# Kernel tuning notes

Measured on AMD Instinct MI355X. Metric: run time of the kernel, lower is better.

The kernel has to match this reference:

```python
import jax, jax.numpy as jnp
import numpy as np

N_NODES_TOTAL = 61440   # B*30
NODES = 30              # per-graph node count (forced by view(-1, 30*128))
E = 491520
IN_CH = 12
CHANS = [128, 512, 128]
KSIZE = 3
FC_OUT = 72             # 12 * 6


def setup_inputs() -> dict:
    key = jax.random.key(0)
    ks = jax.random.split(key, 24)
    d = {}
    d['x'] = jax.random.normal(ks[0], (N_NODES_TOTAL, IN_CH), dtype=jnp.float32)
    d['edge_index'] = jax.random.randint(ks[1], (2, E), 0, N_NODES_TOTAL, dtype=jnp.int64)
    # GCNConv(12, 12): PyG Linear weight [out, in] + bias
    d['gcn_w'] = jax.random.normal(ks[2], (12, 12), dtype=jnp.float32) * (1.0 / np.sqrt(12))
    d['gcn_b'] = jnp.zeros((12,), dtype=jnp.float32)
    # TCN: 3 TemporalBlocks, each uses conv1 (k=3, dilated causal) + 1x1 downsample
    in_c = IN_CH
    for i, out_c in enumerate(CHANS):
        d[f'conv_w{i}'] = jax.random.normal(ks[3 + 4 * i], (out_c, in_c, KSIZE), dtype=jnp.float32) * 0.01
        d[f'conv_b{i}'] = jnp.zeros((out_c,), dtype=jnp.float32)
        d[f'down_w{i}'] = jax.random.normal(ks[4 + 4 * i], (out_c, in_c, 1), dtype=jnp.float32) * 0.01
        d[f'down_b{i}'] = jnp.zeros((out_c,), dtype=jnp.float32)
        in_c = out_c
    d['fc_w'] = jax.random.normal(ks[20], (FC_OUT, CHANS[-1] * NODES), dtype=jnp.float32) * (1.0 / np.sqrt(CHANS[-1] * NODES))
    d['fc_b'] = jnp.zeros((FC_OUT,), dtype=jnp.float32)
    return d


def gcn_conv(x, edge_index, w, b):
    # PyG GCNConv: h = x W^T, add self-loops, sym normalize, scatter-add, + bias
    n = x.shape[0]
    h = x @ w.T
    loop = jnp.arange(n, dtype=edge_index.dtype)
    src = jnp.concatenate([edge_index[0], loop])
    dst = jnp.concatenate([edge_index[1], loop])
    deg = jax.ops.segment_sum(jnp.ones(src.shape[0], dtype=h.dtype), dst, num_segments=n)
    dinv = jnp.where(deg > 0, jax.lax.rsqrt(deg), 0.0)
    norm = dinv[src] * dinv[dst]                       # [E+N]
    out = jax.ops.segment_sum(norm[:, None] * h[src], dst, num_segments=n)
    return out + b


def causal_conv1d(x, w, b, dilation):
    # torch Conv1d(pad=(k-1)*d both sides) + Chomp1d((k-1)*d) == left-pad causal conv
    k = w.shape[-1]
    pad = (k - 1) * dilation
    y = jax.lax.conv_general_dilated(
        x, w, window_strides=(1,), padding=[(pad, 0)],
        rhs_dilation=(dilation,), dimension_numbers=('NCH', 'OIH', 'NCH'))
    return y + b[None, :, None]


def reference(x, edge_index, gcn_w, gcn_b,
              conv_w0, conv_b0, down_w0, down_b0,
              conv_w1, conv_b1, down_w1, down_b1,
              conv_w2, conv_b2, down_w2, down_b2,
              fc_w, fc_b):
    X = gcn_conv(x, edge_index, gcn_w, gcn_b)          # [B*30, 12]
    X = X.reshape(-1, NODES, IN_CH).transpose(0, 2, 1)  # [B, 12, 30]
    blocks = [(conv_w0, conv_b0, down_w0, down_b0),
              (conv_w1, conv_b1, down_w1, down_b1),
              (conv_w2, conv_b2, down_w2, down_b2)]
    for i, (cw, cb, dw, db) in enumerate(blocks):
        dil = 3 ** i
        out = jax.nn.relu(causal_conv1d(X, cw, cb, dil))
        res = causal_conv1d(X, dw, db, 1)              # 1x1 downsample (always in!=out here)
        X = jax.nn.relu(out + res)
    T = jax.nn.relu(X)                                  # [B, 128, 30]
    T = T.reshape(T.shape[0], -1)                       # [B, 3840], channel-major like torch flatten
    return T @ fc_w.T + fc_b                            # [B, 72]
```

## Files before the change

### kernel.cpp

```cpp
#include <hip/hip_runtime.h>
#include <hip/hip_bf16.h>

#define N_NODES 61440
#define NEDGE   491520
#define BATCH   2048
#define TT      30
#define C1      128
#define C2      512
#define C3      128
#define FCK     3840
#define MAXDEG  40

typedef float floatx16 __attribute__((ext_vector_type(16)));
typedef __bf16 bfrag   __attribute__((ext_vector_type(8)));

static __device__ __forceinline__ unsigned short f2bf(float f) {
    unsigned u = __float_as_uint(f);
    u = u + 0x7fffu + ((u >> 16) & 1u);
    return (unsigned short)(u >> 16);
}
static __device__ __forceinline__ bfrag ldf(const void* p) { return *(const bfrag*)p; }
#define MFMA(a, b, c) __builtin_amdgcn_mfma_f32_32x32x16_bf16(a, b, c, 0, 0, 0)

__global__ void k_edges_repack(
        const int* __restrict__ e32, int* __restrict__ cnt,
        unsigned short* __restrict__ eidx,
        const float* __restrict__ cw0, const float* __restrict__ dw0,
        const float* __restrict__ cw1, const float* __restrict__ dw1,
        const float* __restrict__ cw2, const float* __restrict__ dw2,
        const float* __restrict__ fcw,
        float* __restrict__ w0T, float* __restrict__ d0T,
        unsigned short* __restrict__ W1f, unsigned short* __restrict__ D1f,
        unsigned short* __restrict__ W2f, unsigned short* __restrict__ D2f,
        unsigned short* __restrict__ FCWf) {
    if (blockIdx.x < 1920) {
        int i = blockIdx.x * 256 + threadIdx.x;
        bool is64 = (e32[1] == 0) & (e32[3] == 0) & (e32[5] == 0) & (e32[7] == 0);
        int s, d;
        if (is64) { s = e32[2 * i]; d = e32[2 * (NEDGE + i)]; }
        else      { s = e32[i];     d = e32[NEDGE + i]; }
        int slot = atomicAdd(&cnt[d], 1);
        if (slot < MAXDEG) eidx[slot * N_NODES + d] = (unsigned short)s;
        return;
    }
    int i = (blockIdx.x - 1920) * 256 + threadIdx.x;
    if (i < 36 * 128) { int oc = i & 127, r = i >> 7; w0T[i] = cw0[oc * 36 + r]; }
    if (i < 12 * 128) { int oc = i & 127, ic = i >> 7; d0T[i] = dw0[oc * 12 + ic]; }
    if (i < 196608) {
        int pos = i & 511, f = i >> 9;
        int lane = pos >> 3, e = pos & 7;
        int oct = f & 15, q = (f >> 4) & 7, tap = f >> 7;
        int oc = oct * 32 + (lane & 31), ic = q * 16 + (lane >> 5) * 8 + e;
        W1f[i] = f2bf(cw1[(oc * 128 + ic) * 3 + tap]);
    } else if (i < 262144) {
        int j = i - 196608;
        int pos = j & 511, f = j >> 9;
        int lane = pos >> 3, e = pos & 7;
        int oct = f & 15, q = f >> 4;
        int oc = oct * 32 + (lane & 31), ic = q * 16 + (lane >> 5) * 8 + e;
        D1f[j] = f2bf(dw1[oc * 128 + ic]);
    } else if (i < 458752) {
        int j = i - 262144;
        int pos = j & 511, f = j >> 9;
        int lane = pos >> 3, e = pos & 7;
        int oct = f & 3, q = (f >> 2) & 31, tap = f >> 7;
        int oc = oct * 32 + (lane & 31), ic = q * 16 + (lane >> 5) * 8 + e;
        W2f[j] = f2bf(cw2[(oc * 512 + ic) * 3 + tap]);
    } else if (i < 524288) {
        int j = i - 458752;
        int pos = j & 511, f = j >> 9;
        int lane = pos >> 3, e = pos & 7;
        int oct = f & 3, q = f >> 2;
        int oc = oct * 32 + (lane & 31), ic = q * 16 + (lane >> 5) * 8 + e;
        D2f[j] = f2bf(dw2[oc * 512 + ic]);
    } else if (i < 892928) {
        int j = i - 524288;
        int pos = j & 511, f = j >> 9;
        int lane = pos >> 3, e = pos & 7;
        int oct = f % 3, q = f / 3;
        int o = oct * 32 + (lane & 31);
        int k = q * 16 + (lane >> 5) * 8 + e;
        float v = (o < 72) ? fcw[o * 3840 + (k & 127) * 30 + (k >> 7)] : 0.f;
        FCWf[j] = f2bf(v);
    }
}

__global__ __launch_bounds__(256) void k_block0(
        const float* __restrict__ x, const int* __restrict__ cnt,
        const unsigned short* __restrict__ eidx,
        const float* __restrict__ gw, const float* __restrict__ gb,
        const float* __restrict__ w0T, const float* __restrict__ d0T,
        const float* __restrict__ cb0, const float* __restrict__ db0,
        unsigned short* __restrict__ X1b) {
    __shared__ float wl[36 * 128];
    __shared__ float dl[12 * 128];
    __shared__ float cbl[128], dbl[128];
    __shared__ float gwl[144], gbl[12];
    __shared__ float aL[120][12];
    __shared__ float x0[4 * TT * 12];
    __shared__ __align__(16) unsigned short st[2][TT * 136];
    int tid = threadIdx.x;
    int b0 = blockIdx.x * 4;
    for (int i = tid; i < 36 * 128; i += 256) wl[i] = w0T[i];
    for (int i = tid; i < 12 * 128; i += 256) dl[i] = d0T[i];
    if (tid < 128) { cbl[tid] = cb0[tid]; dbl[tid] = db0[tid]; }
    if (tid < 144) gwl[tid] = gw[tid];
    if (tid >= 144 && tid < 156) gbl[tid - 144] = gb[tid - 144];

    {
        int th = tid & 127;
        int grp = tid >> 7;
        if (th < 120) {
            size_t n = (size_t)b0 * TT + th;
            int ne = cnt[n]; if (ne > MAXDEG) ne = MAXDEG;
            float a0 = 0.f, a1 = 0.f, a2 = 0.f, a3 = 0.f, a4 = 0.f, a5 = 0.f;
            for (int j = 0; j < ne; j++) {
                int s = eidx[j * N_NODES + n];
                float di = rsqrtf(1.0f + (float)cnt[s]);
                const float2* xp = (const float2*)(x + (size_t)s * 12 + grp * 6);
                float2 p0 = xp[0], p1 = xp[1], p2 = xp[2];
                a0 += di * p0.x; a1 += di * p0.y;
                a2 += di * p1.x; a3 += di * p1.y;
                a4 += di * p2.x; a5 += di * p2.y;
            }
            float* ap = &aL[th][grp * 6];
            ap[0] = a0; ap[1] = a1; ap[2] = a2; ap[3] = a3; ap[4] = a4; ap[5] = a5;
        }
    }
    __syncthreads();

    if (tid < 120) {
        size_t n = (size_t)b0 * TT + tid;
        float di = rsqrtf(1.0f + (float)cnt[n]);
        float d2 = di * di;
        const float4* xp = (const float4*)(x + n * 12);
        float u[12];
        #pragma unroll
        for (int q = 0; q < 3; q++) {
            float4 xv = xp[q];
            u[q*4+0] = di * aL[tid][q*4+0] + d2 * xv.x;
            u[q*4+1] = di * aL[tid][q*4+1] + d2 * xv.y;
            u[q*4+2] = di * aL[tid][q*4+2] + d2 * xv.z;
            u[q*4+3] = di * aL[tid][q*4+3] + d2 * xv.w;
        }
        #pragma unroll
        for (int c = 0; c < 12; c++) {
            float acc = gbl[c];
            #pragma unroll
            for (int j = 0; j < 12; j++) acc += u[j] * gwl[c * 12 + j];
            x0[tid * 12 + c] = acc;
        }
    }
    __syncthreads();

    int oc = tid & 127, half = tid >> 7;
    float cb = cbl[oc], db = dbl[oc];
    for (int bi = 0; bi < 2; bi++) {
        int bl = bi * 2 + half;
        const float* xb = x0 + bl * (TT * 12);
        float conv[TT], res[TT];
        #pragma unroll
        for (int t = 0; t < TT; t++) { conv[t] = 0.f; res[t] = 0.f; }
        #pragma unroll
        for (int ic = 0; ic < 12; ic++) {
            float w0v = wl[(ic * 3 + 0) * 128 + oc];
            float w1v = wl[(ic * 3 + 1) * 128 + oc];
            float w2v = wl[(ic * 3 + 2) * 128 + oc];
            float dv  = dl[ic * 128 + oc];
            #pragma unroll
            for (int t = 0; t < TT; t++) {
                float xv = xb[t * 12 + ic];
                conv[t] += w2v * xv;
                if (t + 1 < TT) conv[t + 1] += w1v * xv;
                if (t + 2 < TT) conv[t + 2] += w0v * xv;
                res[t] += dv * xv;
            }
        }
        #pragma unroll
        for (int t = 0; t < TT; t++) {
            float o1 = fmaxf(conv[t] + cb, 0.f);
            st[half][t * 136 + oc] = f2bf(fmaxf(o1 + res[t] + db, 0.f));
        }
        __syncthreads();
        for (int idx = tid; idx < 2 * TT * 16; idx += 256) {
            int h = idx / (TT * 16), rem = idx - h * (TT * 16);
            int row = rem >> 4, seg = rem & 15;
            *(uint4*)(X1b + (size_t)((b0 + bi * 2 + h) * TT + row) * 128 + seg * 8) =
                *(const uint4*)(&st[h][row * 136 + seg * 8]);
        }
        __syncthreads();
    }
}

__global__ __launch_bounds__(512, 2) void k_tcn12(
        const unsigned short* __restrict__ X1b,
        const unsigned short* __restrict__ W1f, const unsigned short* __restrict__ D1f,
        const float* __restrict__ cb1, const float* __restrict__ db1,
        const unsigned short* __restrict__ W2f, const unsigned short* __restrict__ D2f,
        const float* __restrict__ cb2, const float* __restrict__ db2,
        unsigned short* __restrict__ X3b) {
    __shared__ __align__(16) unsigned short X1l[61 * 136];
    __shared__ __align__(16) unsigned short X2l[61 * 520];
    const int tid  = threadIdx.x;
    const int lane = tid & 63;
    const int wave = tid >> 6;
    const int tcol = lane & 31;
    const int half = lane >> 5;
    const int b0 = blockIdx.x * 2;

    auto ldw1 = [&](bfrag* dst, int oct, int qc) {
        #pragma unroll
        for (int tap = 0; tap < 3; tap++)
            #pragma unroll
            for (int qq = 0; qq < 4; qq++)
                dst[tap * 4 + qq] =
                    ldf(W1f + (((tap * 8 + qc * 4 + qq) * 16 + oct) << 9) + lane * 8);
        #pragma unroll
        for (int qq = 0; qq < 4; qq++)
            dst[12 + qq] = ldf(D1f + (((qc * 4 + qq) * 16 + oct) << 9) + lane * 8);
    };
    auto ldw2 = [&](bfrag* dst, int oct, int qc) {
        #pragma unroll
        for (int tap = 0; tap < 3; tap++)
            #pragma unroll
            for (int qq = 0; qq < 4; qq++)
                dst[tap * 4 + qq] =
                    ldf(W2f + (((tap * 32 + qc * 4 + qq) * 4 + oct) << 9) + lane * 8);
        #pragma unroll
        for (int qq = 0; qq < 4; qq++)
            dst[12 + qq] = ldf(D2f + (((qc * 4 + qq) * 4 + oct) << 9) + lane * 8);
    };

    for (int idx = tid; idx < 960; idx += 512) {
        int row = idx >> 4, seg = idx & 15;
        *(uint4*)(X1l + row * 136 + seg * 8) =
            *(const uint4*)(X1b + ((size_t)(b0 * 30 + row) << 7) + seg * 8);
    }
    if (tid < 17) *(uint4*)(X1l + 60 * 136 + tid * 8) = make_uint4(0, 0, 0, 0);
    if (tid < 65) *(uint4*)(X2l + 60 * 520 + tid * 8) = make_uint4(0, 0, 0, 0);
    __syncthreads();

    {
        bfrag wf[2][16];
        ldw1(wf[0], wave, 0);
        floatx16 accc[2], accd[2];
        #pragma unroll
        for (int s = 0; s < 4; s++) {
            const int qc = s & 1;
            const int oct = (s >> 1) * 8 + wave;
            if (qc == 0) { accc[0] = 0; accc[1] = 0; accd[0] = 0; accd[1] = 0; }
            if (s < 3)
                ldw1(wf[(s + 1) & 1], ((s + 1) >> 1) * 8 + wave, (s + 1) & 1);
            #pragma unroll
            for (int bl = 0; bl < 2; bl++) {
                bfrag bx[3][4];
                #pragma unroll
                for (int si = 0; si < 3; si++) {
                    int trow = tcol - si * 3;
                    const unsigned short* rp = ((unsigned)trow < 30u)
                        ? (X1l + (bl * 30 + trow) * 136) : (X1l + 60 * 136);
                    #pragma unroll
                    for (int qq = 0; qq < 4; qq++)
                        bx[si][qq] = ldf(rp + (qc * 4 + qq) * 16 + half * 8);
                }
                #pragma unroll
                for (int qq = 0; qq < 4; qq++) {
                    accc[bl] = MFMA(wf[s & 1][8 + qq],  bx[0][qq], accc[bl]);
                    accc[bl] = MFMA(wf[s & 1][4 + qq],  bx[1][qq], accc[bl]);
                    accc[bl] = MFMA(wf[s & 1][qq],      bx[2][qq], accc[bl]);
                    accd[bl] = MFMA(wf[s & 1][12 + qq], bx[0][qq], accd[bl]);
                }
            }
            if (qc == 1 && tcol < 30) {
                #pragma unroll
                for (int bl = 0; bl < 2; bl++) {
                    unsigned short* wp = X2l + (bl * 30 + tcol) * 520 + oct * 32 + half * 4;
                    #pragma unroll
                    for (int gi = 0; gi < 4; gi++) {
                        int ocb = oct * 32 + half * 4 + gi * 8;
                        float4 cbv = *(const float4*)(cb1 + ocb);
                        float4 dbv = *(const float4*)(db1 + ocb);
                        float v0 = fmaxf(fmaxf(accc[bl][gi*4+0] + cbv.x, 0.f) + accd[bl][gi*4+0] + dbv.x, 0.f);
                        float v1 = fmaxf(fmaxf(accc[bl][gi*4+1] + cbv.y, 0.f) + accd[bl][gi*4+1] + dbv.y, 0.f);
                        float v2 = fmaxf(fmaxf(accc[bl][gi*4+2] + cbv.z, 0.f) + accd[bl][gi*4+2] + dbv.z, 0.f);
                        float v3 = fmaxf(fmaxf(accc[bl][gi*4+3] + cbv.w, 0.f) + accd[bl][gi*4+3] + dbv.w, 0.f);
                        unsigned p0 = (unsigned)f2bf(v0) | ((unsigned)f2bf(v1) << 16);
                        unsigned p1 = (unsigned)f2bf(v2) | ((unsigned)f2bf(v3) << 16);
                        *(uint2*)(wp + gi * 8) = make_uint2(p0, p1);
                    }
                }
            }
        }
    }
    __syncthreads();

    {
        const int oct = wave & 3;
        const int bl  = wave >> 2;
        bfrag wf[2][16];
        ldw2(wf[0], oct, 0);
        floatx16 accc, accd;
        accc = 0; accd = 0;
        #pragma unroll
        for (int qc = 0; qc < 8; qc++) {
            if (qc < 7) ldw2(wf[(qc + 1) & 1], oct, qc + 1);
            bfrag bx[3][4];
            #pragma unroll
            for (int si = 0; si < 3; si++) {
                int trow = tcol - si * 9;
                const unsigned short* rp = ((unsigned)trow < 30u)
                    ? (X2l + (bl * 30 + trow) * 520) : (X2l + 60 * 520);
                #pragma unroll
                for (int qq = 0; qq < 4; qq++)
                    bx[si][qq] = ldf(rp + (qc * 4 + qq) * 16 + half * 8);
            }
            #pragma unroll
            for (int qq = 0; qq < 4; qq++) {
                accc = MFMA(wf[qc & 1][8 + qq],  bx[0][qq], accc);
                accc = MFMA(wf[qc & 1][4 + qq],  bx[1][qq], accc);
                accc = MFMA(wf[qc & 1][qq],      bx[2][qq], accc);
                accd = MFMA(wf[qc & 1][12 + qq], bx[0][qq], accd);
            }
        }
        if (tcol < 30) {
            unsigned short* wp = X1l + (bl * 30 + tcol) * 136 + oct * 32 + half * 4;
            #pragma unroll
            for (int gi = 0; gi < 4; gi++) {
                int ocb = oct * 32 + half * 4 + gi * 8;
                float4 cbv = *(const float4*)(cb2 + ocb);
                float4 dbv = *(const float4*)(db2 + ocb);
                float v0 = fmaxf(fmaxf(accc[gi*4+0] + cbv.x, 0.f) + accd[gi*4+0] + dbv.x, 0.f);
                float v1 = fmaxf(fmaxf(accc[gi*4+1] + cbv.y, 0.f) + accd[gi*4+1] + dbv.y, 0.f);
                float v2 = fmaxf(fmaxf(accc[gi*4+2] + cbv.z, 0.f) + accd[gi*4+2] + dbv.z, 0.f);
                float v3 = fmaxf(fmaxf(accc[gi*4+3] + cbv.w, 0.f) + accd[gi*4+3] + dbv.w, 0.f);
                unsigned p0 = (unsigned)f2bf(v0) | ((unsigned)f2bf(v1) << 16);
                unsigned p1 = (unsigned)f2bf(v2) | ((unsigned)f2bf(v3) << 16);
                *(uint2*)(wp + gi * 8) = make_uint2(p0, p1);
            }
        }
    }
    __syncthreads();
    for (int idx = tid; idx < 960; idx += 512) {
        int row = idx >> 4, seg = idx & 15;
        *(uint4*)(X3b + ((size_t)(b0 * 30 + row) << 7) + seg * 8) =
            *(const uint4*)(X1l + row * 136 + seg * 8);
    }
}

__global__ __launch_bounds__(256) void k_fc_mfma(
        const unsigned short* __restrict__ X3b,
        const unsigned short* __restrict__ FCWf,
        unsigned short* __restrict__ P) {
    __shared__ __align__(16) unsigned short xt[128 * 248];
    const int tid  = threadIdx.x;
    const int lane = tid & 63;
    const int wave = tid >> 6;
    const int half = lane >> 5;
    const int bg = blockIdx.x & 15;
    const int kc = blockIdx.x >> 4;

    for (int idx = tid; idx < 128 * 32; idx += 256) {
        int row = idx >> 5, seg = idx & 31;
        if (seg < 30)
            *(uint4*)(xt + row * 248 + seg * 8) =
                *(const uint4*)(X3b + (size_t)(bg * 128 + row) * FCK + kc * 240 + seg * 8);
    }
    __syncthreads();

    const int bl = wave * 32 + (lane & 31);
    floatx16 acc[3];
    acc[0] = 0; acc[1] = 0; acc[2] = 0;
    #pragma unroll
    for (int ql = 0; ql < 15; ql++) {
        int q = kc * 15 + ql;
        bfrag bx = ldf(xt + bl * 248 + ql * 16 + half * 8);
        #pragma unroll
        for (int oct = 0; oct < 3; oct++) {
            bfrag af = ldf(FCWf + ((q * 3 + oct) << 9) + lane * 8);
            acc[oct] = MFMA(af, bx, acc[oct]);
        }
    }
    unsigned short* base = P + (size_t)kc * 96 * BATCH;
    const int b = bg * 128 + bl;
    #pragma unroll
    for (int oct = 0; oct < 3; oct++)
        #pragma unroll
        for (int j = 0; j < 16; j++) {
            int o = oct * 32 + half * 4 + (j >> 2) * 8 + (j & 3);
            base[(size_t)o * BATCH + b] = f2bf(acc[oct][j]);
        }
}

__global__ __launch_bounds__(256) void k_fc_reduce(
        const unsigned short* __restrict__ P, const float* __restrict__ fcb,
        float* __restrict__ out) {
    int j = blockIdx.x * blockDim.x + threadIdx.x;
    int o = j >> 11, b = j & 2047;
    float acc = fcb[o];
    #pragma unroll
    for (int kc = 0; kc < 16; kc++) {
        unsigned u = P[((size_t)kc * 96 + o) * BATCH + b];
        acc += __uint_as_float(u << 16);
    }
    out[b * 72 + o] = acc;
}


extern "C" void kernel_launch(void* const* d_in, const int* in_sizes, int n_in,
                              void* d_out, int out_size, void* d_ws, size_t ws_size,
                              hipStream_t stream) {
    const float* x   = (const float*)d_in[0];
    const int*   e32 = (const int*)  d_in[1];
    const float* gw  = (const float*)d_in[2];
    const float* gb  = (const float*)d_in[3];
    const float* cw0 = (const float*)d_in[4];
    const float* cb0 = (const float*)d_in[5];
    const float* dw0 = (const float*)d_in[6];
    const float* db0 = (const float*)d_in[7];
    const float* cw1 = (const float*)d_in[8];
    const float* cb1 = (const float*)d_in[9];
    const float* dw1 = (const float*)d_in[10];
    const float* db1 = (const float*)d_in[11];
    const float* cw2 = (const float*)d_in[12];
    const float* cb2 = (const float*)d_in[13];
    const float* dw2 = (const float*)d_in[14];
    const float* db2 = (const float*)d_in[15];
    const float* fcw = (const float*)d_in[16];
    const float* fcb = (const float*)d_in[17];

    char* w = (char*)d_ws;
    auto alloc = [&](size_t bytes) {
        char* p = w;
        w += (bytes + 255) & ~(size_t)255;
        return p;
    };
    int*            cnt  = (int*)           alloc(N_NODES * 4);
    unsigned short* eidx = (unsigned short*)alloc((size_t)N_NODES * MAXDEG * 2);
    float* w0T  = (float*)alloc(36 * 128 * 4);
    float* d0T  = (float*)alloc(12 * 128 * 4);
    unsigned short* W1f  = (unsigned short*)alloc(196608 * 2);
    unsigned short* D1f  = (unsigned short*)alloc(65536 * 2);
    unsigned short* W2f  = (unsigned short*)alloc(196608 * 2);
    unsigned short* D2f  = (unsigned short*)alloc(65536 * 2);
    unsigned short* FCWf = (unsigned short*)alloc(368640 * 2);
    unsigned short* X1b  = (unsigned short*)alloc((size_t)BATCH * TT * C1 * 2);
    unsigned short* X3b  = (unsigned short*)alloc((size_t)BATCH * TT * C3 * 2);
    unsigned short* P    = (unsigned short*)alloc((size_t)16 * 96 * BATCH * 2);

    hipMemsetAsync(cnt, 0, N_NODES * 4, stream);
    k_edges_repack<<<1920 + 3488, 256, 0, stream>>>(
        e32, cnt, eidx, cw0, dw0, cw1, dw1, cw2, dw2, fcw,
        w0T, d0T, W1f, D1f, W2f, D2f, FCWf);
    k_block0<<<BATCH / 4, 256, 0, stream>>>(x, cnt, eidx, gw, gb,
                                            w0T, d0T, cb0, db0, X1b);
    k_tcn12<<<BATCH / 2, 512, 0, stream>>>(X1b, W1f, D1f, cb1, db1,
                                           W2f, D2f, cb2, db2, X3b);
    k_fc_mfma<<<256, 256, 0, stream>>>(X3b, FCWf, P);
    k_fc_reduce<<<72 * BATCH / 256, 256, 0, stream>>>(P, fcb, (float*)d_out);
}
```

Before: 170.3 us.

## Split fused TCN blocks 1-2 into two kernels via global bf16 intermediate

The fused k_tcn12 kernel, which held both the 128-channel and 512-channel activations in LDS, is split into k_tcn1 (writes the 512-channel output to a new global X2b buffer) and k_tcn2 (one graph per 256-thread block). Weight fragments are now loaded inside the inner loop instead of being double-buffered in registers. The aim is less LDS and register pressure per block so more waves fit per CU. In exchange it adds a global round trip of about 63 MB of bf16 intermediate data, one more kernel launch, and redundant weight loads across more blocks.

```diff
diff --git a/kernel.cpp b/kernel.cpp
--- a/kernel.cpp
+++ b/kernel.cpp
@@ -192,15 +192,12 @@
     }
 }
 
-__global__ __launch_bounds__(512, 2) void k_tcn12(
+__global__ __launch_bounds__(256, 3) void k_tcn1(
         const unsigned short* __restrict__ X1b,
         const unsigned short* __restrict__ W1f, const unsigned short* __restrict__ D1f,
         const float* __restrict__ cb1, const float* __restrict__ db1,
-        const unsigned short* __restrict__ W2f, const unsigned short* __restrict__ D2f,
-        const float* __restrict__ cb2, const float* __restrict__ db2,
-        unsigned short* __restrict__ X3b) {
+        unsigned short* __restrict__ X2b) {
     __shared__ __align__(16) unsigned short X1l[61 * 136];
-    __shared__ __align__(16) unsigned short X2l[61 * 520];
     const int tid  = threadIdx.x;
     const int lane = tid & 63;
     const int wave = tid >> 6;
@@ -208,142 +205,136 @@
     const int half = lane >> 5;
     const int b0 = blockIdx.x * 2;
 
-    auto ldw1 = [&](bfrag* dst, int oct, int qc) {
-        #pragma unroll
-        for (int tap = 0; tap < 3; tap++)
-            #pragma unroll
-            for (int qq = 0; qq < 4; qq++)
-                dst[tap * 4 + qq] =
-                    ldf(W1f + (((tap * 8 + qc * 4 + qq) * 16 + oct) << 9) + lane * 8);
-        #pragma unroll
-        for (int qq = 0; qq < 4; qq++)
-            dst[12 + qq] = ldf(D1f + (((qc * 4 + qq) * 16 + oct) << 9) + lane * 8);
-    };
-    auto ldw2 = [&](bfrag* dst, int oct, int qc) {
-        #pragma unroll
-        for (int tap = 0; tap < 3; tap++)
-            #pragma unroll
-            for (int qq = 0; qq < 4; qq++)
-                dst[tap * 4 + qq] =
-                    ldf(W2f + (((tap * 32 + qc * 4 + qq) * 4 + oct) << 9) + lane * 8);
-        #pragma unroll
-        for (int qq = 0; qq < 4; qq++)
-            dst[12 + qq] = ldf(D2f + (((qc * 4 + qq) * 4 + oct) << 9) + lane * 8);
-    };
-
-    for (int idx = tid; idx < 960; idx += 512) {
+    for (int idx = tid; idx < 960; idx += 256) {
         int row = idx >> 4, seg = idx & 15;
         *(uint4*)(X1l + row * 136 + seg * 8) =
             *(const uint4*)(X1b + ((size_t)(b0 * 30 + row) << 7) + seg * 8);
     }
     if (tid < 17) *(uint4*)(X1l + 60 * 136 + tid * 8) = make_uint4(0, 0, 0, 0);
-    if (tid < 65) *(uint4*)(X2l + 60 * 520 + tid * 8) = make_uint4(0, 0, 0, 0);
-    __syncthreads();
-
-    {
-        bfrag wf[2][16];
-        ldw1(wf[0], wave, 0);
-        floatx16 accc[2], accd[2];
-        #pragma unroll
-        for (int s = 0; s < 4; s++) {
-            const int qc = s & 1;
-            const int oct = (s >> 1) * 8 + wave;
-            if (qc == 0) { accc[0] = 0; accc[1] = 0; accd[0] = 0; accd[1] = 0; }
-            if (s < 3)
-                ldw1(wf[(s + 1) & 1], ((s + 1) >> 1) * 8 + wave, (s + 1) & 1);
+    __syncthreads();
+
+    floatx16 accc[2], accd[2];
+    #pragma unroll
+    for (int s = 0; s < 8; s++) {
+        const int qc = s & 1;
+        const int oct = (s >> 1) * 4 + wave;
+        if (qc == 0) { accc[0] = 0; accc[1] = 0; accd[0] = 0; accd[1] = 0; }
+        #pragma unroll
+        for (int qq = 0; qq < 4; qq++) {
+            bfrag w2 = ldf(W1f + (((2 * 8 + qc * 4 + qq) * 16 + oct) << 9) + lane * 8);
+            bfrag w1 = ldf(W1f + (((1 * 8 + qc * 4 + qq) * 16 + oct) << 9) + lane * 8);
+            bfrag w0 = ldf(W1f + (((0 * 8 + qc * 4 + qq) * 16 + oct) << 9) + lane * 8);
+            bfrag wd = ldf(D1f + (((qc * 4 + qq) * 16 + oct) << 9) + lane * 8);
+            const int co = (qc * 4 + qq) * 16 + half * 8;
             #pragma unroll
             for (int bl = 0; bl < 2; bl++) {
-                bfrag bx[3][4];
+                int t0 = tcol, t1 = tcol - 3, t2 = tcol - 6;
+                const unsigned short* rp0 = ((unsigned)t0 < 30u)
+                    ? (X1l + (bl * 30 + t0) * 136) : (X1l + 60 * 136);
+                const unsigned short* rp1 = ((unsigned)t1 < 30u)
+                    ? (X1l + (bl * 30 + t1) * 136) : (X1l + 60 * 136);
+                const unsigned short* rp2 = ((unsigned)t2 < 30u)
+                    ? (X1l + (bl * 30 + t2) * 136) : (X1l + 60 * 136);
+                bfrag b0f = ldf(rp0 + co);
+                bfrag b1f = ldf(rp1 + co);
+                bfrag b2f = ldf(rp2 + co);
+                accc[bl] = MFMA(w2, b0f, accc[bl]);
+                accc[bl] = MFMA(w1, b1f, accc[bl]);
+                accc[bl] = MFMA(w0, b2f, accc[bl]);
+                accd[bl] = MFMA(wd, b0f, accd[bl]);
+            }
+        }
+        if (qc == 1 && tcol < 30) {
+            #pragma unroll
+            for (int bl = 0; bl < 2; bl++) {
+                unsigned short* wp = X2b + ((size_t)(b0 + bl) * 30 + tcol) * 512
+                                   + oct * 32 + half * 4;
                 #pragma unroll
-                for (int si = 0; si < 3; si++) {
-                    int trow = tcol - si * 3;
-                    const unsigned short* rp = ((unsigned)trow < 30u)
-                        ? (X1l + (bl * 30 + trow) * 136) : (X1l + 60 * 136);
-                    #pragma unroll
-                    for (int qq = 0; qq < 4; qq++)
-                        bx[si][qq] = ldf(rp + (qc * 4 + qq) * 16 + half * 8);
-                }
-                #pragma unroll
-                for (int qq = 0; qq < 4; qq++) {
-                    accc[bl] = MFMA(wf[s & 1][8 + qq],  bx[0][qq], accc[bl]);
-                    accc[bl] = MFMA(wf[s & 1][4 + qq],  bx[1][qq], accc[bl]);
-                    accc[bl] = MFMA(wf[s & 1][qq],      bx[2][qq], accc[bl]);
-                    accd[bl] = MFMA(wf[s & 1][12 + qq], bx[0][qq], accd[bl]);
+                for (int gi = 0; gi < 4; gi++) {
+                    int ocb = oct * 32 + half * 4 + gi * 8;
+                    float4 cbv = *(const float4*)(cb1 + ocb);
+                    float4 dbv = *(const float4*)(db1 + ocb);
+                    float v0 = fmaxf(fmaxf(accc[bl][gi*4+0] + cbv.x, 0.f) + accd[bl][gi*4+0] + dbv.x, 0.f);
+                    float v1 = fmaxf(fmaxf(accc[bl][gi*4+1] + cbv.y, 0.f) + accd[bl][gi*4+1] + dbv.y, 0.f);
+                    float v2 = fmaxf(fmaxf(accc[bl][gi*4+2] + cbv.z, 0.f) + accd[bl][gi*4+2] + dbv.z, 0.f);
+                    float v3 = fmaxf(fmaxf(accc[bl][gi*4+3] + cbv.w, 0.f) + accd[bl][gi*4+3] + dbv.w, 0.f);
+                    unsigned p0 = (unsigned)f2bf(v0) | ((unsigned)f2bf(v1) << 16);
+                    unsigned p1 = (unsigned)f2bf(v2) | ((unsigned)f2bf(v3) << 16);
+                    *(uint2*)(wp + gi * 8) = make_uint2(p0, p1);
                 }
             }
-            if (qc == 1 && tcol < 30) {
-                #pragma unroll
-                for (int bl = 0; bl < 2; bl++) {
-                    unsigned short* wp = X2l + (bl * 30 + tcol) * 520 + oct * 32 + half * 4;
-                    #pragma unroll
-                    for (int gi = 0; gi < 4; gi++) {
-                        int ocb = oct * 32 + half * 4 + gi * 8;
-                        float4 cbv = *(const float4*)(cb1 + ocb);
-                        float4 dbv = *(const float4*)(db1 + ocb);
-                        float v0 = fmaxf(fmaxf(accc[bl][gi*4+0] + cbv.x, 0.f) + accd[bl][gi*4+0] + dbv.x, 0.f);
-                        float v1 = fmaxf(fmaxf(accc[bl][gi*4+1] + cbv.y, 0.f) + accd[bl][gi*4+1] + dbv.y, 0.f);
-                        float v2 = fmaxf(fmaxf(accc[bl][gi*4+2] + cbv.z, 0.f) + accd[bl][gi*4+2] + dbv.z, 0.f);
-                        float v3 = fmaxf(fmaxf(accc[bl][gi*4+3] + cbv.w, 0.f) + accd[bl][gi*4+3] + dbv.w, 0.f);
-                        unsigned p0 = (unsigned)f2bf(v0) | ((unsigned)f2bf(v1) << 16);
-                        unsigned p1 = (unsigned)f2bf(v2) | ((unsigned)f2bf(v3) << 16);
-                        *(uint2*)(wp + gi * 8) = make_uint2(p0, p1);
-                    }
-                }
-            }
-        }
-    }
-    __syncthreads();
-
-    {
-        const int oct = wave & 3;
-        const int bl  = wave >> 2;
-        bfrag wf[2][16];
-        ldw2(wf[0], oct, 0);
-        floatx16 accc, accd;
-        accc = 0; accd = 0;
-        #pragma unroll
-        for (int qc = 0; qc < 8; qc++) {
-            if (qc < 7) ldw2(wf[(qc + 1) & 1], oct, qc + 1);
-            bfrag bx[3][4];
-            #pragma unroll
-            for (int si = 0; si < 3; si++) {
-                int trow = tcol - si * 9;
-                const unsigned short* rp = ((unsigned)trow < 30u)
-                    ? (X2l + (bl * 30 + trow) * 520) : (X2l + 60 * 520);
-                #pragma unroll
-                for (int qq = 0; qq < 4; qq++)
-                    bx[si][qq] = ldf(rp + (qc * 4 + qq) * 16 + half * 8);
-            }
-            #pragma unroll
-            for (int qq = 0; qq < 4; qq++) {
-                accc = MFMA(wf[qc & 1][8 + qq],  bx[0][qq], accc);
-                accc = MFMA(wf[qc & 1][4 + qq],  bx[1][qq], accc);
-                accc = MFMA(wf[qc & 1][qq],      bx[2][qq], accc);
-                accd = MFMA(wf[qc & 1][12 + qq], bx[0][qq], accd);
-            }
-        }
-        if (tcol < 30) {
-            unsigned short* wp = X1l + (bl * 30 + tcol) * 136 + oct * 32 + half * 4;
-            #pragma unroll
-            for (int gi = 0; gi < 4; gi++) {
-                int ocb = oct * 32 + half * 4 + gi * 8;
-                float4 cbv = *(const float4*)(cb2 + ocb);
-                float4 dbv = *(const float4*)(db2 + ocb);
-                float v0 = fmaxf(fmaxf(accc[gi*4+0] + cbv.x, 0.f) + accd[gi*4+0] + dbv.x, 0.f);
-                float v1 = fmaxf(fmaxf(accc[gi*4+1] + cbv.y, 0.f) + accd[gi*4+1] + dbv.y, 0.f);
-                float v2 = fmaxf(fmaxf(accc[gi*4+2] + cbv.z, 0.f) + accd[gi*4+2] + dbv.z, 0.f);
-                float v3 = fmaxf(fmaxf(accc[gi*4+3] + cbv.w, 0.f) + accd[gi*4+3] + dbv.w, 0.f);
-                unsigned p0 = (unsigned)f2bf(v0) | ((unsigned)f2bf(v1) << 16);
-                unsigned p1 = (unsigned)f2bf(v2) | ((unsigned)f2bf(v3) << 16);
-                *(uint2*)(wp + gi * 8) = make_uint2(p0, p1);
-            }
-        }
-    }
-    __syncthreads();
-    for (int idx = tid; idx < 960; idx += 512) {
+        }
+    }
+}
+
+__global__ __launch_bounds__(256, 4) void k_tcn2(
+        const unsigned short* __restrict__ X2b,
+        const unsigned short* __restrict__ W2f, const unsigned short* __restrict__ D2f,
+        const float* __restrict__ cb2, const float* __restrict__ db2,
+        unsigned short* __restrict__ X3b) {
+    __shared__ __align__(16) unsigned short X2l[31 * 520];
+    const int tid  = threadIdx.x;
+    const int lane = tid & 63;
+    const int wave = tid >> 6;
+    const int tcol = lane & 31;
+    const int half = lane >> 5;
+    const int b = blockIdx.x;
+
+    for (int idx = tid; idx < 1920; idx += 256) {
+        int row = idx >> 6, seg = idx & 63;
+        *(uint4*)(X2l + row * 520 + seg * 8) =
+            *(const uint4*)(X2b + ((size_t)(b * 30 + row) << 9) + seg * 8);
+    }
+    if (tid < 65) *(uint4*)(X2l + 30 * 520 + tid * 8) = make_uint4(0, 0, 0, 0);
+    __syncthreads();
+
+    const int oct = wave;
+    floatx16 accc, accd;
+    accc = 0; accd = 0;
+    #pragma unroll
+    for (int qc = 0; qc < 8; qc++) {
+        #pragma unroll
+        for (int qq = 0; qq < 4; qq++) {
+            bfrag w2 = ldf(W2f + (((2 * 32 + qc * 4 + qq) * 4 + oct) << 9) + lane * 8);
+            bfrag w1 = ldf(W2f + (((1 * 32 + qc * 4 + qq) * 4 + oct) << 9) + lane * 8);
+            bfrag w0 = ldf(W2f + (((0 * 32 + qc * 4 + qq) * 4 + oct) << 9) + lane * 8);
+            bfrag wd = ldf(D2f + (((qc * 4 + qq) * 4 + oct) << 9) + lane * 8);
+            const int co = (qc * 4 + qq) * 16 + half * 8;
+            int t0 = tcol, t1 = tcol - 9, t2 = tcol - 18;
+            const unsigned short* rp0 = ((unsigned)t0 < 30u) ? (X2l + t0 * 520) : (X2l + 30 * 520);
+            const unsigned short* rp1 = ((unsigned)t1 < 30u) ? (X2l + t1 * 520) : (X2l + 30 * 520);
+            const unsigned short* rp2 = ((unsigned)t2 < 30u) ? (X2l + t2 * 520) : (X2l + 30 * 520);
+            bfrag b0f = ldf(rp0 + co);
+            bfrag b1f = ldf(rp1 + co);
+            bfrag b2f = ldf(rp2 + co);
+            accc = MFMA(w2, b0f, accc);
+            accc = MFMA(w1, b1f, accc);
+            accc = MFMA(w0, b2f, accc);
+            accd = MFMA(wd, b0f, accd);
+        }
+    }
+    __syncthreads();
+    if (tcol < 30) {
+        unsigned short* wp = X2l + tcol * 136 + oct * 32 + half * 4;
+        #pragma unroll
+        for (int gi = 0; gi < 4; gi++) {
+            int ocb = oct * 32 + half * 4 + gi * 8;
+            float4 cbv = *(const float4*)(cb2 + ocb);
+            float4 dbv = *(const float4*)(db2 + ocb);
+            float v0 = fmaxf(fmaxf(accc[gi*4+0] + cbv.x, 0.f) + accd[gi*4+0] + dbv.x, 0.f);
+            float v1 = fmaxf(fmaxf(accc[gi*4+1] + cbv.y, 0.f) + accd[gi*4+1] + dbv.y, 0.f);
+            float v2 = fmaxf(fmaxf(accc[gi*4+2] + cbv.z, 0.f) + accd[gi*4+2] + dbv.z, 0.f);
+            float v3 = fmaxf(fmaxf(accc[gi*4+3] + cbv.w, 0.f) + accd[gi*4+3] + dbv.w, 0.f);
+            unsigned p0 = (unsigned)f2bf(v0) | ((unsigned)f2bf(v1) << 16);
+            unsigned p1 = (unsigned)f2bf(v2) | ((unsigned)f2bf(v3) << 16);
+            *(uint2*)(wp + gi * 8) = make_uint2(p0, p1);
+        }
+    }
+    __syncthreads();
+    for (int idx = tid; idx < 480; idx += 256) {
         int row = idx >> 4, seg = idx & 15;
-        *(uint4*)(X3b + ((size_t)(b0 * 30 + row) << 7) + seg * 8) =
-            *(const uint4*)(X1l + row * 136 + seg * 8);
+        *(uint4*)(X3b + ((size_t)(b * 30 + row) << 7) + seg * 8) =
+            *(const uint4*)(X2l + row * 136 + seg * 8);
     }
 }
 
@@ -446,6 +437,7 @@
     unsigned short* X1b  = (unsigned short*)alloc((size_t)BATCH * TT * C1 * 2);
     unsigned short* X3b  = (unsigned short*)alloc((size_t)BATCH * TT * C3 * 2);
     unsigned short* P    = (unsigned short*)alloc((size_t)16 * 96 * BATCH * 2);
+    unsigned short* X2b  = (unsigned short*)alloc((size_t)BATCH * TT * C2 * 2);
 
     hipMemsetAsync(cnt, 0, N_NODES * 4, stream);
     k_edges_repack<<<1920 + 3488, 256, 0, stream>>>(
@@ -453,8 +445,8 @@
         w0T, d0T, W1f, D1f, W2f, D2f, FCWf);
     k_block0<<<BATCH / 4, 256, 0, stream>>>(x, cnt, eidx, gw, gb,
                                             w0T, d0T, cb0, db0, X1b);
-    k_tcn12<<<BATCH / 2, 512, 0, stream>>>(X1b, W1f, D1f, cb1, db1,
-                                           W2f, D2f, cb2, db2, X3b);
+    k_tcn1<<<BATCH / 2, 256, 0, stream>>>(X1b, W1f, D1f, cb1, db1, X2b);
+    k_tcn2<<<BATCH, 256, 0, stream>>>(X2b, W2f, D2f, cb2, db2, X3b);
     k_fc_mfma<<<256, 256, 0, stream>>>(X3b, FCWf, P);
     k_fc_reduce<<<72 * BATCH / 256, 256, 0, stream>>>(P, fcb, (float*)d_out);
 }
```

Measured after the change: 187.5 us. +10.0%, slower.
